# Kernel optimization log

Hardware: AMD Instinct MI355X
Metric: run time of the kernel (lower is better)

## Reference

```python
import jax, jax.numpy as jnp
import numpy as np

N_AGENTS = 3
OBS_DIM = 30
ACT_DIM = 9
HIDDEN = 128
HEADS = 4
HEAD_DIM = HIDDEN // HEADS
BATCH = 131072
NEG_SLOPE = 0.01
MASK_VAL = -1e10


def _leaky(x):
    return jnp.where(x >= 0, x, NEG_SLOPE * x)


def setup_inputs() -> dict:
    key = jax.random.key(0)
    ks = jax.random.split(key, 20)

    def init(k, shape, fan_in):
        return jax.random.normal(k, shape, dtype=jnp.float32) / np.sqrt(fan_in)

    inp = {
        "observations": jax.random.normal(ks[0], (BATCH, N_AGENTS, OBS_DIM), dtype=jnp.float32),
        "actions": jax.random.uniform(ks[1], (BATCH, N_AGENTS, ACT_DIM), dtype=jnp.float32),
        # per-agent embed weights, stacked over agents: [N, in, out] (already transposed vs torch)
        "W_o": init(ks[2], (N_AGENTS, OBS_DIM, HIDDEN), OBS_DIM),
        "b_o": jnp.zeros((N_AGENTS, HIDDEN), dtype=jnp.float32),
        "W_oa": init(ks[3], (N_AGENTS, OBS_DIM + ACT_DIM, HIDDEN), OBS_DIM + ACT_DIM),
        "b_oa": jnp.zeros((N_AGENTS, HIDDEN), dtype=jnp.float32),
        # shared attention projections: [in, out]
        "Wq": init(ks[4], (HIDDEN, HIDDEN), HIDDEN),
        "bq": jnp.zeros((HIDDEN,), dtype=jnp.float32),
        "Wk": init(ks[5], (HIDDEN, HIDDEN), HIDDEN),
        "bk": jnp.zeros((HIDDEN,), dtype=jnp.float32),
        "Wv": init(ks[6], (HIDDEN, HIDDEN), HIDDEN),
        "bv": jnp.zeros((HIDDEN,), dtype=jnp.float32),
        # per-agent critic MLP: Linear(2H->H) + LeakyReLU + Linear(H->A)
        "Wc1": init(ks[7], (N_AGENTS, 2 * HIDDEN, HIDDEN), 2 * HIDDEN),
        "bc1": jnp.zeros((N_AGENTS, HIDDEN), dtype=jnp.float32),
        "Wc2": init(ks[8], (N_AGENTS, HIDDEN, ACT_DIM), HIDDEN),
        "bc2": jnp.zeros((N_AGENTS, ACT_DIM), dtype=jnp.float32),
    }
    return inp


def reference(observations, actions, W_o, b_o, W_oa, b_oa, Wq, bq, Wk, bk, Wv, bv, Wc1, bc1, Wc2, bc2):
    B, N, _ = observations.shape

    # per-agent embeds as a single batched GEMM over the agent axis
    o_emb = _leaky(jnp.einsum('bnd,ndh->bnh', observations, W_o) + b_o)          # [B,N,H]
    oa = jnp.concatenate([observations, actions], axis=-1)                        # [B,N,O+A]
    oa_emb = _leaky(jnp.einsum('bnd,ndh->bnh', oa, W_oa) + b_oa)                  # [B,N,H]

    # shared Q/K/V projections, split heads -> [B, heads, N, head_dim]
    def heads(x):
        return x.reshape(B, N, HEADS, HEAD_DIM).transpose(0, 2, 1, 3)

    Q = heads(o_emb @ Wq + bq)
    K = heads(oa_emb @ Wk + bk)
    V = heads(oa_emb @ Wv + bv)

    scores = jnp.einsum('bhnd,bhmd->bhnm', Q, K) / np.sqrt(HEAD_DIM).astype(np.float32)
    mask = jnp.where(jnp.eye(N, dtype=bool), jnp.float32(MASK_VAL), 0.0)          # diag masked
    attn = jax.nn.softmax(scores + mask, axis=-1)
    attn_out = jnp.einsum('bhnm,bhmd->bhnd', attn, V)
    attn_out = attn_out.transpose(0, 2, 1, 3).reshape(B, N, HIDDEN)               # [B,N,H]

    # per-agent critics, again batched over the agent axis
    c_in = jnp.concatenate([o_emb, attn_out], axis=-1)                            # [B,N,2H]
    h = _leaky(jnp.einsum('bnd,ndh->bnh', c_in, Wc1) + bc1)
    q_values = jnp.einsum('bnh,nha->bna', h, Wc2) + bc2                           # [B,N,A]
    return q_values
```

## Files before the change

### kernel.cpp

```cpp
#include <hip/hip_runtime.h>
#include <stdint.h>

typedef unsigned short u16;
typedef unsigned int u32;
typedef __attribute__((ext_vector_type(8))) short short8;
typedef __attribute__((ext_vector_type(4))) float floatx4;

#define BATCH   131072
#define NA      3
#define OBS     30
#define ACTD    9
#define HID     128
#define HEADS   4
#define HD      32
#define MB      16
#define ROWS    (MB*NA)
#define LDC     136
#define LDOA    72
#define QSCALE  0.17677669529663687f
#define NTHREADS 512

#define OFF_WO    0
#define OFF_WOA   12288
#define OFF_WQ    36864
#define OFF_WK    53248
#define OFF_WV    69632
#define OFF_WC1   86016
#define OFF_WC2   184320
#define PRE_TOTAL 190464

#define MFMA(A,B,C) __builtin_amdgcn_mfma_f32_16x16x32_bf16((A),(B),(C),0,0,0)

__device__ __forceinline__ u16 f2bf(float f) {
    union { float f; u32 u; } v; v.f = f;
    return (u16)((v.u + 0x8000u) >> 16);
}
__device__ __forceinline__ u32 pk_bf16(float a, float b) {
    union { float f; u32 u; } x, y; x.f = a; y.f = b;
    return ((x.u + 0x8000u) >> 16) | ((y.u + 0x8000u) & 0xffff0000u);
}
__device__ __forceinline__ float lo16f(u32 w) { union { u32 u; float f; } v; v.u = w << 16; return v.f; }
__device__ __forceinline__ float hi16f(u32 w) { union { u32 u; float f; } v; v.u = w & 0xffff0000u; return v.f; }
__device__ __forceinline__ float leaky(float x) { return x >= 0.f ? x : 0.01f * x; }

__global__ void prepack_kernel(const float* __restrict__ Wo,  const float* __restrict__ Woa,
                               const float* __restrict__ Wq,  const float* __restrict__ Wk,
                               const float* __restrict__ Wv,  const float* __restrict__ Wc1,
                               const float* __restrict__ Wc2, u16* __restrict__ out) {
    int i = blockIdx.x * blockDim.x + threadIdx.x;
    if (i >= PRE_TOTAL) return;
    const float* src; int K, KT, perA, base, Nsrc, Nlim; float scl = 1.f;
    if (i < OFF_WOA)      { src = Wo;  K = 30;  KT = 1; perA = 4096;  base = OFF_WO;  Nsrc = 128; Nlim = 128; }
    else if (i < OFF_WQ)  { src = Woa; K = 39;  KT = 2; perA = 8192;  base = OFF_WOA; Nsrc = 128; Nlim = 128; }
    else if (i < OFF_WK)  { src = Wq;  K = 128; KT = 4; perA = 16384; base = OFF_WQ;  Nsrc = 128; Nlim = 128; scl = QSCALE; }
    else if (i < OFF_WV)  { src = Wk;  K = 128; KT = 4; perA = 16384; base = OFF_WK;  Nsrc = 128; Nlim = 128; }
    else if (i < OFF_WC1) { src = Wv;  K = 128; KT = 4; perA = 16384; base = OFF_WV;  Nsrc = 128; Nlim = 128; }
    else if (i < OFF_WC2) { src = Wc1; K = 256; KT = 8; perA = 32768; base = OFF_WC1; Nsrc = 128; Nlim = 128; }
    else                  { src = Wc2; K = 128; KT = 4; perA = 2048;  base = OFF_WC2; Nsrc = 9;   Nlim = 9;   }
    int j = i - base;
    int agent = j / perA;
    int r = j - agent * perA;
    int e = r & 7, lane = (r >> 3) & 63, fk = r >> 9;
    int kt = fk % KT, nt = fk / KT;
    int n = nt * 16 + (lane & 15);
    int k = kt * 32 + (lane >> 4) * 8 + e;
    u16 v = 0;
    if (k < K && n < Nlim) v = f2bf(src[(agent * K + k) * Nsrc + n] * scl);
    out[i] = v;
}

__global__ __launch_bounds__(NTHREADS, 6) void fused_kernel(
    const float* __restrict__ obs, const float* __restrict__ act,
    const float* __restrict__ b_o, const float* __restrict__ b_oa,
    const float* __restrict__ bq,  const float* __restrict__ bk_, const float* __restrict__ bv,
    const float* __restrict__ bc1, const float* __restrict__ bc2,
    const u16* __restrict__ pre, float* __restrict__ out)
{
    __shared__ __align__(16) u16 s_mem[4 * ROWS * LDC];
    u16* s_oemb  = s_mem;
    u16* s_oaemb = s_mem + ROWS * LDC;
    u16* s_bufA  = s_mem + 2 * ROWS * LDC;
    u16* s_bufB  = s_mem + 3 * ROWS * LDC;

    const int tid  = threadIdx.x;
    const int wave = tid >> 6, lane = tid & 63;
    const int l15  = lane & 15, quad = lane >> 4;
    const int b0   = blockIdx.x * MB;
    const short8* preV = (const short8*)pre;

    const int nh2 = wave & 3;
    const int ag0 = wave >> 2;
    const int ag2 = (wave + 4) >> 2;
    const int pb0 = OFF_WO / 8 + ag0 * 512;
    const int pb1 = (wave < 4) ? (OFF_WO / 8 + 2 * 512) : (OFF_WOA / 8);
    const int kt1n = (wave < 4) ? 1 : 2;
    const int pb2 = OFF_WOA / 8 + ag2 * 1024;
    const int proj = wave >> 2;

    for (int g = tid; g < ROWS * 15; g += NTHREADS) {
        int r = g / 15, s = g - r * 15;
        int n = r / MB, bl = r - n * MB;
        const float* src = &obs[((b0 + bl) * NA + n) * OBS + 2 * s];
        *(u32*)&s_bufA[n * (MB * LDOA) + bl * LDOA + 2 * s] = pk_bf16(src[0], src[1]);
    }
    for (int g = tid; g < ROWS * 5; g += NTHREADS) {
        int r = g / 5, s = g - r * 5;
        int n = r / MB, bl = r - n * MB;
        const float* src = &act[((b0 + bl) * NA + n) * ACTD + 2 * s];
        float v0 = src[0], v1 = (s < 4) ? src[1] : 0.f;
        *(u32*)&s_bufA[n * (MB * LDOA) + bl * LDOA + 30 + 2 * s] = pk_bf16(v0, v1);
    }
    for (int g = tid; g < ROWS * 3; g += NTHREADS) {
        int r = g / 3, s = g - r * 3;
        int n = r / MB, bl = r - n * MB;
        *(uint4*)&s_bufA[n * (MB * LDOA) + bl * LDOA + 40 + 8 * s] = make_uint4(0, 0, 0, 0);
    }
    __syncthreads();

    {
        short8 w1_00 = preV[pb0 + (nh2 * 2 + 0) * 64 + lane];
        short8 w1_01 = preV[pb0 + (nh2 * 2 + 1) * 64 + lane];
        short8 w1_100 = preV[pb1 + ((nh2 * 2 + 0) * kt1n + 0) * 64 + lane];
        short8 w1_101 = preV[pb1 + ((nh2 * 2 + 0) * kt1n + 1) * 64 + lane];
        short8 w1_110 = preV[pb1 + ((nh2 * 2 + 1) * kt1n + 0) * 64 + lane];
        short8 w1_111 = preV[pb1 + ((nh2 * 2 + 1) * kt1n + 1) * 64 + lane];
        short8 w1_200 = preV[pb2 + ((nh2 * 2 + 0) * 2 + 0) * 64 + lane];
        short8 w1_201 = preV[pb2 + ((nh2 * 2 + 0) * 2 + 1) * 64 + lane];
        short8 w1_210 = preV[pb2 + ((nh2 * 2 + 1) * 2 + 0) * 64 + lane];
        short8 w1_211 = preV[pb2 + ((nh2 * 2 + 1) * 2 + 1) * 64 + lane];
        const float* bj0 = b_o + ag0 * HID;
        const float* bj1 = (wave < 4) ? (b_o + 2 * HID) : b_oa;
        const float* bj2 = b_oa + ag2 * HID;
        float b1_00 = bj0[(nh2 * 2 + 0) * 16 + l15];
        float b1_01 = bj0[(nh2 * 2 + 1) * 16 + l15];
        float b1_10 = bj1[(nh2 * 2 + 0) * 16 + l15];
        float b1_11 = bj1[(nh2 * 2 + 1) * 16 + l15];
        float b1_20 = bj2[(nh2 * 2 + 0) * 16 + l15];
        float b1_21 = bj2[(nh2 * 2 + 1) * 16 + l15];
        int col0 = nh2 * 32 + l15;
        {
            short8 a = *(const short8*)&s_bufA[ag0 * (MB * LDOA) + l15 * LDOA + quad * 8];
            floatx4 acc0 = {}, acc1 = {};
            acc0 = MFMA(a, w1_00, acc0);
            acc1 = MFMA(a, w1_01, acc1);
            #pragma unroll
            for (int rg = 0; rg < 4; rg++) {
                int m = quad * 4 + rg;
                s_oemb[(m * NA + ag0) * LDC + col0]      = f2bf(leaky(acc0[rg] + b1_00));
                s_oemb[(m * NA + ag0) * LDC + col0 + 16] = f2bf(leaky(acc1[rg] + b1_01));
            }
        }
        {
            int ag1 = (wave < 4) ? 2 : 0;
            short8 a0 = *(const short8*)&s_bufA[ag1 * (MB * LDOA) + l15 * LDOA + quad * 8];
            floatx4 acc0 = {}, acc1 = {};
            acc0 = MFMA(a0, w1_100, acc0);
            acc1 = MFMA(a0, w1_110, acc1);
            if (wave >= 4) {
                short8 a1 = *(const short8*)&s_bufA[ag1 * (MB * LDOA) + l15 * LDOA + 32 + quad * 8];
                acc0 = MFMA(a1, w1_101, acc0);
                acc1 = MFMA(a1, w1_111, acc1);
            }
            u16* dst = (wave < 4) ? s_oemb : s_oaemb;
            #pragma unroll
            for (int rg = 0; rg < 4; rg++) {
                int m = quad * 4 + rg;
                dst[(m * NA + ag1) * LDC + col0]      = f2bf(leaky(acc0[rg] + b1_10));
                dst[(m * NA + ag1) * LDC + col0 + 16] = f2bf(leaky(acc1[rg] + b1_11));
            }
        }
        {
            short8 a0 = *(const short8*)&s_bufA[ag2 * (MB * LDOA) + l15 * LDOA + quad * 8];
            short8 a1 = *(const short8*)&s_bufA[ag2 * (MB * LDOA) + l15 * LDOA + 32 + quad * 8];
            floatx4 acc0 = {}, acc1 = {};
            acc0 = MFMA(a0, w1_200, acc0);
            acc0 = MFMA(a1, w1_201, acc0);
            acc1 = MFMA(a0, w1_210, acc1);
            acc1 = MFMA(a1, w1_211, acc1);
            #pragma unroll
            for (int rg = 0; rg < 4; rg++) {
                int m = quad * 4 + rg;
                s_oaemb[(m * NA + ag2) * LDC + col0]      = f2bf(leaky(acc0[rg] + b1_20));
                s_oaemb[(m * NA + ag2) * LDC + col0 + 16] = f2bf(leaky(acc1[rg] + b1_21));
            }
        }
    }
    __syncthreads();

    {
        const int pbqk = (proj ? OFF_WK : OFF_WQ) / 8;
        const float* bqk = proj ? bk_ : bq;
        const float bscl = proj ? 1.f : QSCALE;
        short8 w2_00 = preV[pbqk + ((nh2 * 2 + 0) * 4 + 0) * 64 + lane];
        short8 w2_01 = preV[pbqk + ((nh2 * 2 + 0) * 4 + 1) * 64 + lane];
        short8 w2_02 = preV[pbqk + ((nh2 * 2 + 0) * 4 + 2) * 64 + lane];
        short8 w2_03 = preV[pbqk + ((nh2 * 2 + 0) * 4 + 3) * 64 + lane];
        short8 w2_10 = preV[pbqk + ((nh2 * 2 + 1) * 4 + 0) * 64 + lane];
        short8 w2_11 = preV[pbqk + ((nh2 * 2 + 1) * 4 + 1) * 64 + lane];
        short8 w2_12 = preV[pbqk + ((nh2 * 2 + 1) * 4 + 2) * 64 + lane];
        short8 w2_13 = preV[pbqk + ((nh2 * 2 + 1) * 4 + 3) * 64 + lane];
        float b2_0 = bqk[(nh2 * 2 + 0) * 16 + l15] * bscl;
        float b2_1 = bqk[(nh2 * 2 + 1) * 16 + l15] * bscl;
        const u16* Abuf = proj ? s_oaemb : s_oemb;
        u16* dst = proj ? s_bufB : s_bufA;
        int col0 = nh2 * 32 + l15;
        for (int mt = 0; mt < 3; mt++) {
            short8 xa0 = *(const short8*)&Abuf[(mt * 16 + l15) * LDC + 0  + quad * 8];
            short8 xa1 = *(const short8*)&Abuf[(mt * 16 + l15) * LDC + 32 + quad * 8];
            short8 xa2 = *(const short8*)&Abuf[(mt * 16 + l15) * LDC + 64 + quad * 8];
            short8 xa3 = *(const short8*)&Abuf[(mt * 16 + l15) * LDC + 96 + quad * 8];
            floatx4 acc0 = {}, acc1 = {};
            acc0 = MFMA(xa0, w2_00, acc0); acc0 = MFMA(xa1, w2_01, acc0);
            acc0 = MFMA(xa2, w2_02, acc0); acc0 = MFMA(xa3, w2_03, acc0);
            acc1 = MFMA(xa0, w2_10, acc1); acc1 = MFMA(xa1, w2_11, acc1);
            acc1 = MFMA(xa2, w2_12, acc1); acc1 = MFMA(xa3, w2_13, acc1);
            #pragma unroll
            for (int rg = 0; rg < 4; rg++) {
                int m = mt * 16 + quad * 4 + rg;
                dst[m * LDC + col0]      = f2bf(acc0[rg] + b2_0);
                dst[m * LDC + col0 + 16] = f2bf(acc1[rg] + b2_1);
            }
        }
    }
    __syncthreads();

    float2 prob = make_float2(0.f, 0.f);
    int e3 = 0, h3 = 0, n3 = 0, m30 = 0, m31 = 0, half3 = 0;
    const bool attn_thread = (tid < 2 * MB * HEADS * NA);
    if (attn_thread) {
        int job = tid >> 1;
        half3 = tid & 1;
        int r = job;
        e3 = r / (HEADS * NA); r -= e3 * HEADS * NA; h3 = r / NA; n3 = r - h3 * NA;
        m30 = (n3 == 0) ? 1 : 0;
        m31 = (n3 == 2) ? 1 : 2;
        const int co = h3 * HD + half3 * 16;
        const uint4* qp  = (const uint4*)&s_bufA[(e3 * NA + n3) * LDC + co];
        const uint4* kp0 = (const uint4*)&s_bufB[(e3 * NA + m30) * LDC + co];
        const uint4* kp1 = (const uint4*)&s_bufB[(e3 * NA + m31) * LDC + co];
        float s0 = 0.f, s1 = 0.f;
        #pragma unroll
        for (int c = 0; c < 2; c++) {
            uint4 qw = qp[c], aw = kp0[c], bw = kp1[c];
            u32 qv[4] = {qw.x, qw.y, qw.z, qw.w};
            u32 av[4] = {aw.x, aw.y, aw.z, aw.w};
            u32 bv_[4] = {bw.x, bw.y, bw.z, bw.w};
            #pragma unroll
            for (int j = 0; j < 4; j++) {
                float ql = lo16f(qv[j]), qh = hi16f(qv[j]);
                s0 += ql * lo16f(av[j]) + qh * hi16f(av[j]);
                s1 += ql * lo16f(bv_[j]) + qh * hi16f(bv_[j]);
            }
        }
        s0 += __shfl_xor(s0, 1);
        s1 += __shfl_xor(s1, 1);
        float mx = fmaxf(s0, s1);
        float p0 = __expf(s0 - mx), p1 = __expf(s1 - mx);
        float inv = 1.f / (p0 + p1);
        prob = make_float2(p0 * inv, p1 * inv);
    }
    __syncthreads();

    {
        short8 w3_0 = preV[OFF_WV / 8 + (wave * 4 + 0) * 64 + lane];
        short8 w3_1 = preV[OFF_WV / 8 + (wave * 4 + 1) * 64 + lane];
        short8 w3_2 = preV[OFF_WV / 8 + (wave * 4 + 2) * 64 + lane];
        short8 w3_3 = preV[OFF_WV / 8 + (wave * 4 + 3) * 64 + lane];
        float b3v = bv[wave * 16 + l15];
        int colv = wave * 16 + l15;
        for (int mt = 0; mt < 3; mt++) {
            short8 xa0 = *(const short8*)&s_oaemb[(mt * 16 + l15) * LDC + 0  + quad * 8];
            short8 xa1 = *(const short8*)&s_oaemb[(mt * 16 + l15) * LDC + 32 + quad * 8];
            short8 xa2 = *(const short8*)&s_oaemb[(mt * 16 + l15) * LDC + 64 + quad * 8];
            short8 xa3 = *(const short8*)&s_oaemb[(mt * 16 + l15) * LDC + 96 + quad * 8];
            floatx4 acc = {};
            acc = MFMA(xa0, w3_0, acc); acc = MFMA(xa1, w3_1, acc);
            acc = MFMA(xa2, w3_2, acc); acc = MFMA(xa3, w3_3, acc);
            #pragma unroll
            for (int rg = 0; rg < 4; rg++) {
                int m = mt * 16 + quad * 4 + rg;
                s_bufA[m * LDC + colv] = f2bf(acc[rg] + b3v);
            }
        }
    }
    __syncthreads();

    if (attn_thread) {
        const int co = h3 * HD + half3 * 16;
        const uint4* v0p = (const uint4*)&s_bufA[(e3 * NA + m30) * LDC + co];
        const uint4* v1p = (const uint4*)&s_bufA[(e3 * NA + m31) * LDC + co];
        uint4* dst = (uint4*)&s_oaemb[(e3 * NA + n3) * LDC + co];
        #pragma unroll
        for (int c = 0; c < 2; c++) {
            uint4 aw = v0p[c], bw = v1p[c], ow;
            u32 av[4] = {aw.x, aw.y, aw.z, aw.w};
            u32 bv_[4] = {bw.x, bw.y, bw.z, bw.w};
            u32 ov[4];
            #pragma unroll
            for (int j = 0; j < 4; j++) {
                float lo = prob.x * lo16f(av[j]) + prob.y * lo16f(bv_[j]);
                float hi = prob.x * hi16f(av[j]) + prob.y * hi16f(bv_[j]);
                ov[j] = pk_bf16(lo, hi);
            }
            ow.x = ov[0]; ow.y = ov[1]; ow.z = ov[2]; ow.w = ov[3];
            dst[c] = ow;
        }
    }
    __syncthreads();

    {
        int colc = wave * 16 + l15;
        float b4_0 = bc1[0 * HID + wave * 16 + l15];
        float b4_1 = bc1[1 * HID + wave * 16 + l15];
        float b4_2 = bc1[2 * HID + wave * 16 + l15];
        {
            short8 w0 = preV[OFF_WC1 / 8 + 0 * 4096 + (wave * 8 + 0) * 64 + lane];
            short8 w1 = preV[OFF_WC1 / 8 + 0 * 4096 + (wave * 8 + 1) * 64 + lane];
            short8 w2 = preV[OFF_WC1 / 8 + 0 * 4096 + (wave * 8 + 2) * 64 + lane];
            short8 w3 = preV[OFF_WC1 / 8 + 0 * 4096 + (wave * 8 + 3) * 64 + lane];
            short8 w4 = preV[OFF_WC1 / 8 + 0 * 4096 + (wave * 8 + 4) * 64 + lane];
            short8 w5 = preV[OFF_WC1 / 8 + 0 * 4096 + (wave * 8 + 5) * 64 + lane];
            short8 w6 = preV[OFF_WC1 / 8 + 0 * 4096 + (wave * 8 + 6) * 64 + lane];
            short8 w7 = preV[OFF_WC1 / 8 + 0 * 4096 + (wave * 8 + 7) * 64 + lane];
            floatx4 acc = {};
            short8 a;
            a = *(const short8*)&s_oemb [(l15 * NA + 0) * LDC + 0  + quad * 8]; acc = MFMA(a, w0, acc);
            a = *(const short8*)&s_oemb [(l15 * NA + 0) * LDC + 32 + quad * 8]; acc = MFMA(a, w1, acc);
            a = *(const short8*)&s_oemb [(l15 * NA + 0) * LDC + 64 + quad * 8]; acc = MFMA(a, w2, acc);
            a = *(const short8*)&s_oemb [(l15 * NA + 0) * LDC + 96 + quad * 8]; acc = MFMA(a, w3, acc);
            a = *(const short8*)&s_oaemb[(l15 * NA + 0) * LDC + 0  + quad * 8]; acc = MFMA(a, w4, acc);
            a = *(const short8*)&s_oaemb[(l15 * NA + 0) * LDC + 32 + quad * 8]; acc = MFMA(a, w5, acc);
            a = *(const short8*)&s_oaemb[(l15 * NA + 0) * LDC + 64 + quad * 8]; acc = MFMA(a, w6, acc);
            a = *(const short8*)&s_oaemb[(l15 * NA + 0) * LDC + 96 + quad * 8]; acc = MFMA(a, w7, acc);
            #pragma unroll
            for (int rg = 0; rg < 4; rg++) {
                int m = quad * 4 + rg;
                s_bufB[(m * NA + 0) * LDC + colc] = f2bf(leaky(acc[rg] + b4_0));
            }
        }
        {
            short8 w0 = preV[OFF_WC1 / 8 + 1 * 4096 + (wave * 8 + 0) * 64 + lane];
            short8 w1 = preV[OFF_WC1 / 8 + 1 * 4096 + (wave * 8 + 1) * 64 + lane];
            short8 w2 = preV[OFF_WC1 / 8 + 1 * 4096 + (wave * 8 + 2) * 64 + lane];
            short8 w3 = preV[OFF_WC1 / 8 + 1 * 4096 + (wave * 8 + 3) * 64 + lane];
            short8 w4 = preV[OFF_WC1 / 8 + 1 * 4096 + (wave * 8 + 4) * 64 + lane];
            short8 w5 = preV[OFF_WC1 / 8 + 1 * 4096 + (wave * 8 + 5) * 64 + lane];
            short8 w6 = preV[OFF_WC1 / 8 + 1 * 4096 + (wave * 8 + 6) * 64 + lane];
            short8 w7 = preV[OFF_WC1 / 8 + 1 * 4096 + (wave * 8 + 7) * 64 + lane];
            floatx4 acc = {};
            short8 a;
            a = *(const short8*)&s_oemb [(l15 * NA + 1) * LDC + 0  + quad * 8]; acc = MFMA(a, w0, acc);
            a = *(const short8*)&s_oemb [(l15 * NA + 1) * LDC + 32 + quad * 8]; acc = MFMA(a, w1, acc);
            a = *(const short8*)&s_oemb [(l15 * NA + 1) * LDC + 64 + quad * 8]; acc = MFMA(a, w2, acc);
            a = *(const short8*)&s_oemb [(l15 * NA + 1) * LDC + 96 + quad * 8]; acc = MFMA(a, w3, acc);
            a = *(const short8*)&s_oaemb[(l15 * NA + 1) * LDC + 0  + quad * 8]; acc = MFMA(a, w4, acc);
            a = *(const short8*)&s_oaemb[(l15 * NA + 1) * LDC + 32 + quad * 8]; acc = MFMA(a, w5, acc);
            a = *(const short8*)&s_oaemb[(l15 * NA + 1) * LDC + 64 + quad * 8]; acc = MFMA(a, w6, acc);
            a = *(const short8*)&s_oaemb[(l15 * NA + 1) * LDC + 96 + quad * 8]; acc = MFMA(a, w7, acc);
            #pragma unroll
            for (int rg = 0; rg < 4; rg++) {
                int m = quad * 4 + rg;
                s_bufB[(m * NA + 1) * LDC + colc] = f2bf(leaky(acc[rg] + b4_1));
            }
        }
        {
            short8 w0 = preV[OFF_WC1 / 8 + 2 * 4096 + (wave * 8 + 0) * 64 + lane];
            short8 w1 = preV[OFF_WC1 / 8 + 2 * 4096 + (wave * 8 + 1) * 64 + lane];
            short8 w2 = preV[OFF_WC1 / 8 + 2 * 4096 + (wave * 8 + 2) * 64 + lane];
            short8 w3 = preV[OFF_WC1 / 8 + 2 * 4096 + (wave * 8 + 3) * 64 + lane];
            short8 w4 = preV[OFF_WC1 / 8 + 2 * 4096 + (wave * 8 + 4) * 64 + lane];
            short8 w5 = preV[OFF_WC1 / 8 + 2 * 4096 + (wave * 8 + 5) * 64 + lane];
            short8 w6 = preV[OFF_WC1 / 8 + 2 * 4096 + (wave * 8 + 6) * 64 + lane];
            short8 w7 = preV[OFF_WC1 / 8 + 2 * 4096 + (wave * 8 + 7) * 64 + lane];
            floatx4 acc = {};
            short8 a;
            a = *(const short8*)&s_oemb [(l15 * NA + 2) * LDC + 0  + quad * 8]; acc = MFMA(a, w0, acc);
            a = *(const short8*)&s_oemb [(l15 * NA + 2) * LDC + 32 + quad * 8]; acc = MFMA(a, w1, acc);
            a = *(const short8*)&s_oemb [(l15 * NA + 2) * LDC + 64 + quad * 8]; acc = MFMA(a, w2, acc);
            a = *(const short8*)&s_oemb [(l15 * NA + 2) * LDC + 96 + quad * 8]; acc = MFMA(a, w3, acc);
            a = *(const short8*)&s_oaemb[(l15 * NA + 2) * LDC + 0  + quad * 8]; acc = MFMA(a, w4, acc);
            a = *(const short8*)&s_oaemb[(l15 * NA + 2) * LDC + 32 + quad * 8]; acc = MFMA(a, w5, acc);
            a = *(const short8*)&s_oaemb[(l15 * NA + 2) * LDC + 64 + quad * 8]; acc = MFMA(a, w6, acc);
            a = *(const short8*)&s_oaemb[(l15 * NA + 2) * LDC + 96 + quad * 8]; acc = MFMA(a, w7, acc);
            #pragma unroll
            for (int rg = 0; rg < 4; rg++) {
                int m = quad * 4 + rg;
                s_bufB[(m * NA + 2) * LDC + colc] = f2bf(leaky(acc[rg] + b4_2));
            }
        }
    }
    __syncthreads();

    if (wave < NA) {
        int agent = wave;
        short8 w5_0 = preV[OFF_WC2 / 8 + agent * 256 + 0 * 64 + lane];
        short8 w5_1 = preV[OFF_WC2 / 8 + agent * 256 + 1 * 64 + lane];
        short8 w5_2 = preV[OFF_WC2 / 8 + agent * 256 + 2 * 64 + lane];
        short8 w5_3 = preV[OFF_WC2 / 8 + agent * 256 + 3 * 64 + lane];
        floatx4 acc = {};
        short8 a;
        a = *(const short8*)&s_bufB[(l15 * NA + agent) * LDC + 0  + quad * 8]; acc = MFMA(a, w5_0, acc);
        a = *(const short8*)&s_bufB[(l15 * NA + agent) * LDC + 32 + quad * 8]; acc = MFMA(a, w5_1, acc);
        a = *(const short8*)&s_bufB[(l15 * NA + agent) * LDC + 64 + quad * 8]; acc = MFMA(a, w5_2, acc);
        a = *(const short8*)&s_bufB[(l15 * NA + agent) * LDC + 96 + quad * 8]; acc = MFMA(a, w5_3, acc);
        if (l15 < ACTD) {
            float b5v = bc2[agent * ACTD + l15];
            #pragma unroll
            for (int rg = 0; rg < 4; rg++) {
                int m = quad * 4 + rg;
                out[((b0 + m) * NA + agent) * ACTD + l15] = acc[rg] + b5v;
            }
        }
    }
}

extern "C" void kernel_launch(void* const* d_in, const int* in_sizes, int n_in,
                              void* d_out, int out_size, void* d_ws, size_t ws_size,
                              hipStream_t stream) {
    const float* obs = (const float*)d_in[0];
    const float* act = (const float*)d_in[1];
    const float* Wo  = (const float*)d_in[2];
    const float* bo  = (const float*)d_in[3];
    const float* Woa = (const float*)d_in[4];
    const float* boa = (const float*)d_in[5];
    const float* Wq  = (const float*)d_in[6];
    const float* bq  = (const float*)d_in[7];
    const float* Wk  = (const float*)d_in[8];
    const float* bk  = (const float*)d_in[9];
    const float* Wv  = (const float*)d_in[10];
    const float* bv  = (const float*)d_in[11];
    const float* Wc1 = (const float*)d_in[12];
    const float* bc1 = (const float*)d_in[13];
    const float* Wc2 = (const float*)d_in[14];
    const float* bc2 = (const float*)d_in[15];
    u16* pre = (u16*)d_ws;

    prepack_kernel<<<(PRE_TOTAL + 255) / 256, 256, 0, stream>>>(Wo, Woa, Wq, Wk, Wv, Wc1, Wc2, pre);
    fused_kernel<<<BATCH / MB, NTHREADS, 0, stream>>>(obs, act, bo, boa, bq, bk, bv, bc1, bc2, pre,
                                                      (float*)d_out);
}
```

Baseline: 258.1 us.

## Compute V projection alongside Q/K stage and hold results in registers

Moves the V projection MFMAs into the Q/K projection stage, so each wave computes its V tile there and keeps the packed bf16 results in registers until after the softmax stage, where they are written to shared memory. The goal is to overlap V compute with Q/K work, take the V GEMM off the critical path between the two attention phases, and reuse the already-loaded oa_emb fragments for waves doing K. The cost is higher register pressure from the extra weight fragments and live packed values, which could lower occupancy. It also assumes a pk_bf16 helper exists.

```diff
diff --git a/kernel.cpp b/kernel.cpp
--- a/kernel.cpp
+++ b/kernel.cpp
@@ -187,6 +187,7 @@
     }
     __syncthreads();
 
+    u32 vpk0a, vpk0b, vpk1a, vpk1b, vpk2a, vpk2b;
     {
         const int pbqk = (proj ? OFF_WK : OFF_WQ) / 8;
         const float* bqk = proj ? bk_ : bq;
@@ -199,28 +200,51 @@
         short8 w2_11 = preV[pbqk + ((nh2 * 2 + 1) * 4 + 1) * 64 + lane];
         short8 w2_12 = preV[pbqk + ((nh2 * 2 + 1) * 4 + 2) * 64 + lane];
         short8 w2_13 = preV[pbqk + ((nh2 * 2 + 1) * 4 + 3) * 64 + lane];
+        short8 w3_0 = preV[OFF_WV / 8 + (wave * 4 + 0) * 64 + lane];
+        short8 w3_1 = preV[OFF_WV / 8 + (wave * 4 + 1) * 64 + lane];
+        short8 w3_2 = preV[OFF_WV / 8 + (wave * 4 + 2) * 64 + lane];
+        short8 w3_3 = preV[OFF_WV / 8 + (wave * 4 + 3) * 64 + lane];
         float b2_0 = bqk[(nh2 * 2 + 0) * 16 + l15] * bscl;
         float b2_1 = bqk[(nh2 * 2 + 1) * 16 + l15] * bscl;
+        float b3v = bv[wave * 16 + l15];
         const u16* Abuf = proj ? s_oaemb : s_oemb;
         u16* dst = proj ? s_bufB : s_bufA;
         int col0 = nh2 * 32 + l15;
-        for (int mt = 0; mt < 3; mt++) {
-            short8 xa0 = *(const short8*)&Abuf[(mt * 16 + l15) * LDC + 0  + quad * 8];
-            short8 xa1 = *(const short8*)&Abuf[(mt * 16 + l15) * LDC + 32 + quad * 8];
-            short8 xa2 = *(const short8*)&Abuf[(mt * 16 + l15) * LDC + 64 + quad * 8];
-            short8 xa3 = *(const short8*)&Abuf[(mt * 16 + l15) * LDC + 96 + quad * 8];
-            floatx4 acc0 = {}, acc1 = {};
-            acc0 = MFMA(xa0, w2_00, acc0); acc0 = MFMA(xa1, w2_01, acc0);
-            acc0 = MFMA(xa2, w2_02, acc0); acc0 = MFMA(xa3, w2_03, acc0);
-            acc1 = MFMA(xa0, w2_10, acc1); acc1 = MFMA(xa1, w2_11, acc1);
-            acc1 = MFMA(xa2, w2_12, acc1); acc1 = MFMA(xa3, w2_13, acc1);
-            #pragma unroll
-            for (int rg = 0; rg < 4; rg++) {
-                int m = mt * 16 + quad * 4 + rg;
-                dst[m * LDC + col0]      = f2bf(acc0[rg] + b2_0);
-                dst[m * LDC + col0 + 16] = f2bf(acc1[rg] + b2_1);
-            }
-        }
+
+#define S2_MT(MT, VPA, VPB) { \
+        short8 xa0 = *(const short8*)&Abuf[((MT) * 16 + l15) * LDC + 0  + quad * 8]; \
+        short8 xa1 = *(const short8*)&Abuf[((MT) * 16 + l15) * LDC + 32 + quad * 8]; \
+        short8 xa2 = *(const short8*)&Abuf[((MT) * 16 + l15) * LDC + 64 + quad * 8]; \
+        short8 xa3 = *(const short8*)&Abuf[((MT) * 16 + l15) * LDC + 96 + quad * 8]; \
+        floatx4 acc0 = {}, acc1 = {}; \
+        acc0 = MFMA(xa0, w2_00, acc0); acc0 = MFMA(xa1, w2_01, acc0); \
+        acc0 = MFMA(xa2, w2_02, acc0); acc0 = MFMA(xa3, w2_03, acc0); \
+        acc1 = MFMA(xa0, w2_10, acc1); acc1 = MFMA(xa1, w2_11, acc1); \
+        acc1 = MFMA(xa2, w2_12, acc1); acc1 = MFMA(xa3, w2_13, acc1); \
+        short8 va0, va1, va2, va3; \
+        if (proj) { va0 = xa0; va1 = xa1; va2 = xa2; va3 = xa3; } \
+        else { \
+            va0 = *(const short8*)&s_oaemb[((MT) * 16 + l15) * LDC + 0  + quad * 8]; \
+            va1 = *(const short8*)&s_oaemb[((MT) * 16 + l15) * LDC + 32 + quad * 8]; \
+            va2 = *(const short8*)&s_oaemb[((MT) * 16 + l15) * LDC + 64 + quad * 8]; \
+            va3 = *(const short8*)&s_oaemb[((MT) * 16 + l15) * LDC + 96 + quad * 8]; \
+        } \
+        floatx4 vacc = {}; \
+        vacc = MFMA(va0, w3_0, vacc); vacc = MFMA(va1, w3_1, vacc); \
+        vacc = MFMA(va2, w3_2, vacc); vacc = MFMA(va3, w3_3, vacc); \
+        VPA = pk_bf16(vacc[0] + b3v, vacc[1] + b3v); \
+        VPB = pk_bf16(vacc[2] + b3v, vacc[3] + b3v); \
+        _Pragma("unroll") \
+        for (int rg = 0; rg < 4; rg++) { \
+            int m = (MT) * 16 + quad * 4 + rg; \
+            dst[m * LDC + col0]      = f2bf(acc0[rg] + b2_0); \
+            dst[m * LDC + col0 + 16] = f2bf(acc1[rg] + b2_1); \
+        } }
+
+        S2_MT(0, vpk0a, vpk0b)
+        S2_MT(1, vpk1a, vpk1b)
+        S2_MT(2, vpk2a, vpk2b)
+#undef S2_MT
     }
     __syncthreads();
 
@@ -262,26 +286,22 @@
     __syncthreads();
 
     {
-        short8 w3_0 = preV[OFF_WV / 8 + (wave * 4 + 0) * 64 + lane];
-        short8 w3_1 = preV[OFF_WV / 8 + (wave * 4 + 1) * 64 + lane];
-        short8 w3_2 = preV[OFF_WV / 8 + (wave * 4 + 2) * 64 + lane];
-        short8 w3_3 = preV[OFF_WV / 8 + (wave * 4 + 3) * 64 + lane];
-        float b3v = bv[wave * 16 + l15];
         int colv = wave * 16 + l15;
-        for (int mt = 0; mt < 3; mt++) {
-            short8 xa0 = *(const short8*)&s_oaemb[(mt * 16 + l15) * LDC + 0  + quad * 8];
-            short8 xa1 = *(const short8*)&s_oaemb[(mt * 16 + l15) * LDC + 32 + quad * 8];
-            short8 xa2 = *(const short8*)&s_oaemb[(mt * 16 + l15) * LDC + 64 + quad * 8];
-            short8 xa3 = *(const short8*)&s_oaemb[(mt * 16 + l15) * LDC + 96 + quad * 8];
-            floatx4 acc = {};
-            acc = MFMA(xa0, w3_0, acc); acc = MFMA(xa1, w3_1, acc);
-            acc = MFMA(xa2, w3_2, acc); acc = MFMA(xa3, w3_3, acc);
-            #pragma unroll
-            for (int rg = 0; rg < 4; rg++) {
-                int m = mt * 16 + quad * 4 + rg;
-                s_bufA[m * LDC + colv] = f2bf(acc[rg] + b3v);
-            }
-        }
+        u16* vb = &s_bufA[(quad * 4) * LDC + colv];
+        vb[0 * LDC] = (u16)(vpk0a & 0xffff);
+        vb[1 * LDC] = (u16)(vpk0a >> 16);
+        vb[2 * LDC] = (u16)(vpk0b & 0xffff);
+        vb[3 * LDC] = (u16)(vpk0b >> 16);
+        u16* vb1 = vb + 16 * LDC;
+        vb1[0 * LDC] = (u16)(vpk1a & 0xffff);
+        vb1[1 * LDC] = (u16)(vpk1a >> 16);
+        vb1[2 * LDC] = (u16)(vpk1b & 0xffff);
+        vb1[3 * LDC] = (u16)(vpk1b >> 16);
+        u16* vb2 = vb + 32 * LDC;
+        vb2[0 * LDC] = (u16)(vpk2a & 0xffff);
+        vb2[1 * LDC] = (u16)(vpk2a >> 16);
+        vb2[2 * LDC] = (u16)(vpk2b & 0xffff);
+        vb2[3 * LDC] = (u16)(vpk2b >> 16);
     }
     __syncthreads();
 
```

Result: slower. 359.1 us (+39.1%).
